# Optimization experiments

Hardware: AMD Instinct MI355X
Metric: run time of the kernel (lower is better)

The kernel has to match this reference:

```python
import jax, jax.numpy as jnp
import numpy as np
from jax.scipy.special import logsumexp

N_STATES = 64
N_OBS = 10000
BATCH = 256
T_MAX = 2048


def setup_inputs() -> dict:
    key = jax.random.key(0)
    k1, k2, k3, k4, k5 = jax.random.split(key, 5)
    x = jax.random.randint(k1, (BATCH, T_MAX), 0, N_OBS, dtype=jnp.int64 if jax.config.jax_enable_x64 else jnp.int32)
    T = jax.random.randint(k2, (BATCH,), 1, T_MAX + 1, dtype=x.dtype)  # lengths in [1, T_MAX]
    pi = jnp.zeros((N_STATES,), dtype=jnp.float32)
    unnormalized_transition_matrix = jax.random.normal(k3, (N_STATES, N_STATES), dtype=jnp.float32)
    unnormalized_emission_matrix = jax.random.normal(k4, (N_STATES, N_OBS), dtype=jnp.float32)
    return {
        "x": x,
        "T": T,
        "pi": pi,
        "unnormalized_transition_matrix": unnormalized_transition_matrix,
        "unnormalized_emission_matrix": unnormalized_emission_matrix,
    }


def reference(x, T, pi, unnormalized_transition_matrix, unnormalized_emission_matrix):
    # log p(x) via the log-domain forward algorithm.
    log_pi = jax.nn.log_softmax(pi, axis=0)                                  # [N]
    log_A = jax.nn.log_softmax(unnormalized_transition_matrix, axis=0)       # [N, N], A[i,k] = p(i | k)-style per torch dim=0
    log_E = jax.nn.log_softmax(unnormalized_emission_matrix, axis=1)         # [N, M]

    # emissions[b, t, n] = log_E[n, x[b, t]]  (gather once, not per step)
    emis = log_E.T[x]                                                        # [B, Tm, N]

    alpha0 = emis[:, 0, :] + log_pi                                          # [B, N]

    def step(alpha, e_t):
        # new_alpha[b, i] = e_t[b, i] + logsumexp_k (log_A[i, k] + alpha[b, k])
        new = e_t + logsumexp(log_A[None, :, :] + alpha[:, None, :], axis=2)
        return new, new

    _, alphas = jax.lax.scan(step, alpha0, jnp.swapaxes(emis[:, 1:, :], 0, 1))  # [Tm-1, B, N]
    log_alpha = jnp.concatenate([alpha0[None], alphas], axis=0)              # [Tm, B, N]

    log_sums = logsumexp(log_alpha, axis=2).T                                # [B, Tm]
    idx = (T - 1).astype(jnp.int32)[:, None]
    log_probs = jnp.take_along_axis(log_sums, idx, axis=1)                   # [B, 1]
    return log_probs
```

## Files before the change

kernel.cpp:

```cpp
#include <hip/hip_runtime.h>
#include <math.h>

#define NS   64
#define NOBS 10000
#define NB   256
#define TMAX 2048

#define PIP_OFF 0
#define ASW_OFF 64
#define LSE_OFF (64 + 4096)
#define ET_OFF  (64 + 4096 + 64)

__device__ __forceinline__ float wsum64(float v) {
  v += __shfl_xor(v, 1);
  v += __shfl_xor(v, 2);
  v += __shfl_xor(v, 4);
  v += __shfl_xor(v, 8);
  v += __shfl_xor(v, 16);
  v += __shfl_xor(v, 32);
  return v;
}

#define DPPROR(S, N)                                                           \
  __int_as_float(__builtin_amdgcn_update_dpp(                                  \
      0, __float_as_int(S), 0x120 + (N), 0xF, 0xF, true))

__global__ __launch_bounds__(64) void prep_small(const float* __restrict__ pi,
                                                 const float* __restrict__ A,
                                                 float* __restrict__ ws) {
  const int l = threadIdx.x;
  const int r = l & 15, c = l >> 4;
  float p = pi[l];
  float m = p;
  m = fmaxf(m, __shfl_xor(m, 1));
  m = fmaxf(m, __shfl_xor(m, 2));
  m = fmaxf(m, __shfl_xor(m, 4));
  m = fmaxf(m, __shfl_xor(m, 8));
  m = fmaxf(m, __shfl_xor(m, 16));
  m = fmaxf(m, __shfl_xor(m, 32));
  float ex = expf(p - m);
  float s = wsum64(ex);
  ws[PIP_OFF + l] = ex / s;

  __shared__ float Ap[NS * NS];
  float cm = -3.0e38f;
  for (int i = 0; i < NS; ++i) cm = fmaxf(cm, A[i * NS + l]);
  float cs = 0.f;
  for (int i = 0; i < NS; ++i) cs += expf(A[i * NS + l] - cm);
  float inv = 1.0f / cs;
  for (int i = 0; i < NS; ++i) Ap[i * NS + l] = expf(A[i * NS + l] - cm) * inv;
  __syncthreads();

  const int probe = __builtin_amdgcn_update_dpp(0, l, 0x121, 0xF, 0xF, true);
  const int dir = ((probe & 15) == ((r - 1) & 15)) ? 1 : -1;

  for (int g = 0; g < 4; ++g)
    for (int j = 0; j < 16; ++j)
      ws[ASW_OFF + l * 64 + g * 16 + j] =
          Ap[(r + 16 * g) * NS + (16 * c + ((r - dir * j) & 15))];
}

__global__ __launch_bounds__(256) void emis_lse(const float* __restrict__ E,
                                                float* __restrict__ ws) {
  const int s = blockIdx.x;
  const float* row = E + (size_t)s * NOBS;
  __shared__ float red[4];
  float m = -3.0e38f;
  for (int o = threadIdx.x; o < NOBS; o += 256) m = fmaxf(m, row[o]);
  m = fmaxf(m, __shfl_xor(m, 1));
  m = fmaxf(m, __shfl_xor(m, 2));
  m = fmaxf(m, __shfl_xor(m, 4));
  m = fmaxf(m, __shfl_xor(m, 8));
  m = fmaxf(m, __shfl_xor(m, 16));
  m = fmaxf(m, __shfl_xor(m, 32));
  const int wid = threadIdx.x >> 6;
  if ((threadIdx.x & 63) == 0) red[wid] = m;
  __syncthreads();
  m = fmaxf(fmaxf(red[0], red[1]), fmaxf(red[2], red[3]));
  __syncthreads();
  float sum = 0.f;
  for (int o = threadIdx.x; o < NOBS; o += 256) sum += expf(row[o] - m);
  sum = wsum64(sum);
  if ((threadIdx.x & 63) == 0) red[wid] = sum;
  __syncthreads();
  if (threadIdx.x == 0)
    ws[LSE_OFF + s] = m + logf(red[0] + red[1] + red[2] + red[3]);
}

__global__ __launch_bounds__(256) void emis_fill(const float* __restrict__ E,
                                                 float* __restrict__ ws) {
  const int idx = blockIdx.x * 256 + threadIdx.x;
  if (idx >= NS * NOBS) return;
  const int s = idx & 63;
  const int obs = idx >> 6;
  ws[ET_OFF + idx] = expf(E[(size_t)s * NOBS + obs] - ws[LSE_OFF + s]);
}


#define PIN8(i)                                                                \
  asm volatile("" : "+v"(aw[(i)]), "+v"(aw[(i) + 1]), "+v"(aw[(i) + 2]),       \
                    "+v"(aw[(i) + 3]), "+v"(aw[(i) + 4]), "+v"(aw[(i) + 5]),   \
                    "+v"(aw[(i) + 6]), "+v"(aw[(i) + 7]))
#define PIN_AW() do { PIN8(0); PIN8(8); PIN8(16); PIN8(24);                    \
                      PIN8(32); PIN8(40); PIN8(48); PIN8(56); } while (0)

#define STAGE_CHUNK(XS, HALF) do {                                             \
    _Pragma("unroll")                                                          \
    for (int k_ = 0; k_ < 64; ++k_) {                                          \
      const int xt_ = __builtin_amdgcn_readlane((XS), k_);                     \
      const float* gp_ = ET + ((size_t)(unsigned)xt_ << 6) + lane;             \
      __builtin_amdgcn_global_load_lds(gp_, &ebuf[(((HALF) << 6) + k_) << 6],  \
                                       4, 0, 0);                               \
    } } while (0)

#define EREAD(DST, ADDR, IMM)                                                  \
  asm volatile("ds_read_b32 %0, %1 offset:" #IMM : "=v"(DST) : "v"(ADDR))

#define STEP(u, EC) do {                                                       \
    const int t_ = t0 + (u);                                                   \
    const float e_ = EC[(u)];                                                  \
    float es_;                                                                 \
    if (((u) & 1) != 0) {               \
      const unsigned srf_ = __builtin_amdgcn_readfirstlane(__float_as_uint(s));\
      const int se_ = (int)((srf_ >> 23) & 0xFFu) - 127;                       \
      es_ = e_ * __uint_as_float((unsigned)(127 - se_) << 23);                 \
      E2 += se_;                                                               \
    } else { es_ = e_; }                                                       \
    float rot[16];                                                             \
    rot[0] = s;                                                                \
    rot[1] = DPPROR(s, 1);   rot[2] = DPPROR(s, 2);   rot[3] = DPPROR(s, 3);   \
    rot[4] = DPPROR(s, 4);   rot[5] = DPPROR(s, 5);   rot[6] = DPPROR(s, 6);   \
    rot[7] = DPPROR(s, 7);   rot[8] = DPPROR(s, 8);   rot[9] = DPPROR(s, 9);   \
    rot[10] = DPPROR(s, 10); rot[11] = DPPROR(s, 11); rot[12] = DPPROR(s, 12); \
    rot[13] = DPPROR(s, 13); rot[14] = DPPROR(s, 14); rot[15] = DPPROR(s, 15); \
    float q0a_ = 0.f, q1a_ = 0.f, q2a_ = 0.f, q3a_ = 0.f;                      \
    float q0b_ = 0.f, q1b_ = 0.f, q2b_ = 0.f, q3b_ = 0.f;                      \
    _Pragma("unroll")                                                          \
    for (int j_ = 0; j_ < 8; ++j_) {                                           \
      q0a_ = fmaf(aw[j_],      rot[j_], q0a_);                                 \
      q1a_ = fmaf(aw[16 + j_], rot[j_], q1a_);                                 \
      q2a_ = fmaf(aw[32 + j_], rot[j_], q2a_);                                 \
      q3a_ = fmaf(aw[48 + j_], rot[j_], q3a_);                                 \
      q0b_ = fmaf(aw[8 + j_],  rot[8 + j_], q0b_);                             \
      q1b_ = fmaf(aw[24 + j_], rot[8 + j_], q1b_);                             \
      q2b_ = fmaf(aw[40 + j_], rot[8 + j_], q2b_);                             \
      q3b_ = fmaf(aw[56 + j_], rot[8 + j_], q3b_);                             \
    }                                                                          \
    const float q0_ = q0a_ + q0b_;                                             \
    const float q1_ = q1a_ + q1b_;                                             \
    const float q2_ = q2a_ + q2b_;                                             \
    const float q3_ = q3a_ + q3b_;                                             \
      \
    float em_ = c1m ? q0_ : q2_;                                   \
    float en_ = c1m ? q1_ : q3_;                                   \
    float emc_, enc_;                                                          \
    asm("v_mov_b32 %0, %1" : "=v"(emc_) : "v"(em_));                           \
    asm("v_mov_b32 %0, %1" : "=v"(enc_) : "v"(en_));                           \
    asm("v_permlane32_swap_b32 %0, %1" : "+v"(em_), "+v"(emc_));               \
    asm("v_permlane32_swap_b32 %0, %1" : "+v"(en_), "+v"(enc_));               \
    const float pm_ = inA32 ? em_ : emc_;       \
    const float pn_ = inA32 ? en_ : enc_;       \
    const float ka_ = c1m ? q2_ : q0_;                  \
    const float kb_ = c1m ? q3_ : q1_;                  \
    const float ua_ = ka_ + pm_;                                               \
    const float ub_ = kb_ + pn_;                                               \
                         \
    float gv_ = c0m ? ua_ : ub_;                                               \
    float gvc_;                                                                \
    asm("v_mov_b32 %0, %1" : "=v"(gvc_) : "v"(gv_));                           \
    asm("v_permlane16_swap_b32 %0, %1" : "+v"(gv_), "+v"(gvc_));               \
    const float pg_ = inA16 ? gv_ : gvc_;         \
    const float kp_ = c0m ? ub_ : ua_;                                         \
    const float fin_ = kp_ + pg_;                                              \
    const float w_ = es_ * ((t_ == 0) ? pip : fin_);                           \
    if (t_ == Tn - 1) { vs = w_; e2s = E2; }                                   \
    s = w_;                                                                    \
  } while (0)

#define GROUP(T0, ECUR, ENXT) do {                                             \
    const int t0 = (T0);                                                       \
    { const unsigned ea_ =                                                     \
          ebase + ((unsigned)(((t0 + 4) & 127)) << 8) + ((unsigned)lane << 2); \
      EREAD(ENXT[0], ea_, 0);   EREAD(ENXT[1], ea_, 256);                      \
      EREAD(ENXT[2], ea_, 512); EREAD(ENXT[3], ea_, 768); }                    \
    asm volatile("s_waitcnt lgkmcnt(4)");                                      \
    __builtin_amdgcn_sched_barrier(0);                                         \
    STEP(0, ECUR); STEP(1, ECUR); STEP(2, ECUR); STEP(3, ECUR);                \
  } while (0)

__global__ void __attribute__((amdgpu_flat_work_group_size(64, 64)))
__attribute__((amdgpu_waves_per_eu(1, 1)))
hmm_fwd(const int* __restrict__ x, const int* __restrict__ T,
        const float* __restrict__ ws, float* __restrict__ out) {
  const int lane = threadIdx.x;
  const int b = blockIdx.x;
  const int cgrp = lane >> 4;
  const bool c0m = (cgrp & 1) != 0;
  const bool c1m = (cgrp & 2) != 0;
  const float* __restrict__ ET = ws + ET_OFF;
  const int* __restrict__ xb = x + (size_t)b * TMAX;
  const int Tn = T[b];

  __shared__ __align__(16) float ebuf[128 * 64];
  const unsigned ebase = (unsigned)(size_t)ebuf;

  bool inA32, inA16;
  {
    float qa = __int_as_float(lane), qb;
    asm("v_mov_b32 %0, %1" : "=v"(qb) : "v"(qa));
    asm("v_permlane32_swap_b32 %0, %1" : "+v"(qa), "+v"(qb));
    inA32 = (__float_as_int(qa) == (lane ^ 32));
    float pa = __int_as_float(lane), pb;
    asm("v_mov_b32 %0, %1" : "=v"(pb) : "v"(pa));
    asm("v_permlane16_swap_b32 %0, %1" : "+v"(pa), "+v"(pb));
    inA16 = (__float_as_int(pa) == (lane ^ 16));
  }

  float aw[NS];
  {
    const float4* ar = (const float4*)(ws + ASW_OFF + lane * NS);
#pragma unroll
    for (int q = 0; q < 16; ++q) {
      float4 f = ar[q];
      aw[4 * q + 0] = f.x; aw[4 * q + 1] = f.y;
      aw[4 * q + 2] = f.z; aw[4 * q + 3] = f.w;
    }
  }
  PIN_AW();

  const float pip = ws[PIP_OFF + lane];

  int xcur = xb[lane];
  STAGE_CHUNK(xcur, 0);
  int xnext = xb[64 + lane];
  asm volatile("s_waitcnt vmcnt(0)" ::: "memory");

  float eA[4], eB[4];
  {
    const unsigned ea_ = ebase + ((unsigned)lane << 2);
    EREAD(eA[0], ea_, 0);   EREAD(eA[1], ea_, 256);
    EREAD(eA[2], ea_, 512); EREAD(eA[3], ea_, 768);
  }

  float s = 1.0f;
  float vs = 0.f;
  int E2 = 0, e2s = 0;

  const int nch = (Tn + 63) >> 6;
  for (int c = 0; c < nch; ++c) {
    const int tb = c << 6;
    if (c + 1 < TMAX / 64) STAGE_CHUNK(xnext, (c + 1) & 1);
    xnext = ((c + 2) < TMAX / 64) ? xb[((c + 2) << 6) + lane] : 0;
#pragma unroll 1
    for (int gp = 0; gp < 7; ++gp) {
      GROUP(tb + (gp << 3), eA, eB);
      GROUP(tb + (gp << 3) + 4, eB, eA);
    }
    GROUP(tb + 56, eA, eB);
    asm volatile("s_waitcnt vmcnt(0)" ::: "memory");
    GROUP(tb + 60, eB, eA);
  }

  const float sf = wsum64(vs);
  if (lane == 0) {
    const double lp = (double)logf(sf) + (double)e2s * 0.6931471805599453;
    out[b] = (float)lp;
  }
}

extern "C" void kernel_launch(void* const* d_in, const int* in_sizes, int n_in,
                              void* d_out, int out_size, void* d_ws, size_t ws_size,
                              hipStream_t stream) {
  const int*   x  = (const int*)d_in[0];
  const int*   T  = (const int*)d_in[1];
  const float* pi = (const float*)d_in[2];
  const float* A  = (const float*)d_in[3];
  const float* E  = (const float*)d_in[4];
  float* out = (float*)d_out;
  float* ws  = (float*)d_ws;

  prep_small<<<1, 64, 0, stream>>>(pi, A, ws);
  emis_lse<<<NS, 256, 0, stream>>>(E, ws);
  emis_fill<<<(NS * NOBS + 255) / 256, 256, 0, stream>>>(E, ws);
  hmm_fwd<<<NB, 64, 0, stream>>>(x, T, ws, out);
}
```

Measured before the change: 399.8 us.

## Permute transition weights to drop selects, single FMA chain, rarer renormalization

Reorders the per-lane transition weight layout (row block c^m2) so the cross-lane reduction after the DPP matvec can use the partial sums directly, without the per-step select instructions. The two split FMA accumulator chains are merged into one chain per output, and the exponent renormalization now runs once per four steps instead of every other step. The t==0 case is peeled into a separate first chunk, which removes the per-step pip select. A single longer FMA chain lengthens the dependency latency, and less frequent rescaling makes overflow or underflow more likely.

```diff
diff --git a/kernel.cpp b/kernel.cpp
--- a/kernel.cpp
+++ b/kernel.cpp
@@ -54,10 +54,10 @@
   const int probe = __builtin_amdgcn_update_dpp(0, l, 0x121, 0xF, 0xF, true);
   const int dir = ((probe & 15) == ((r - 1) & 15)) ? 1 : -1;
 
-  for (int g = 0; g < 4; ++g)
+  for (int m2 = 0; m2 < 4; ++m2)
     for (int j = 0; j < 16; ++j)
-      ws[ASW_OFF + l * 64 + g * 16 + j] =
-          Ap[(r + 16 * g) * NS + (16 * c + ((r - dir * j) & 15))];
+      ws[ASW_OFF + l * 64 + m2 * 16 + j] =
+          Ap[(r + 16 * (c ^ m2)) * NS + (16 * c + ((r - dir * j) & 15))];
 }
 
 __global__ __launch_bounds__(256) void emis_lse(const float* __restrict__ E,
@@ -120,7 +120,7 @@
     const int t_ = t0 + (u);                                                   \
     const float e_ = EC[(u)];                                                  \
     float es_;                                                                 \
-    if (((u) & 1) != 0) {               \
+    if ((u) == 3) {                     \
       const unsigned srf_ = __builtin_amdgcn_readfirstlane(__float_as_uint(s));\
       const int se_ = (int)((srf_ >> 23) & 0xFFu) - 127;                       \
       es_ = e_ * __uint_as_float((unsigned)(127 - se_) << 23);                 \
@@ -133,46 +133,35 @@
     rot[7] = DPPROR(s, 7);   rot[8] = DPPROR(s, 8);   rot[9] = DPPROR(s, 9);   \
     rot[10] = DPPROR(s, 10); rot[11] = DPPROR(s, 11); rot[12] = DPPROR(s, 12); \
     rot[13] = DPPROR(s, 13); rot[14] = DPPROR(s, 14); rot[15] = DPPROR(s, 15); \
-    float q0a_ = 0.f, q1a_ = 0.f, q2a_ = 0.f, q3a_ = 0.f;                      \
-    float q0b_ = 0.f, q1b_ = 0.f, q2b_ = 0.f, q3b_ = 0.f;                      \
+         \
+    float q0_ = aw[0]  * rot[0];                                               \
+    float q1_ = aw[16] * rot[0];                                               \
+    float q2_ = aw[32] * rot[0];                                               \
+    float q3_ = aw[48] * rot[0];                                               \
     _Pragma("unroll")                                                          \
-    for (int j_ = 0; j_ < 8; ++j_) {                                           \
-      q0a_ = fmaf(aw[j_],      rot[j_], q0a_);                                 \
-      q1a_ = fmaf(aw[16 + j_], rot[j_], q1a_);                                 \
-      q2a_ = fmaf(aw[32 + j_], rot[j_], q2a_);                                 \
-      q3a_ = fmaf(aw[48 + j_], rot[j_], q3a_);                                 \
-      q0b_ = fmaf(aw[8 + j_],  rot[8 + j_], q0b_);                             \
-      q1b_ = fmaf(aw[24 + j_], rot[8 + j_], q1b_);                             \
-      q2b_ = fmaf(aw[40 + j_], rot[8 + j_], q2b_);                             \
-      q3b_ = fmaf(aw[56 + j_], rot[8 + j_], q3b_);                             \
+    for (int j_ = 1; j_ < 16; ++j_) {                                          \
+      q0_ = fmaf(aw[j_],      rot[j_], q0_);                                   \
+      q1_ = fmaf(aw[16 + j_], rot[j_], q1_);                                   \
+      q2_ = fmaf(aw[32 + j_], rot[j_], q2_);                                   \
+      q3_ = fmaf(aw[48 + j_], rot[j_], q3_);                                   \
     }                                                                          \
-    const float q0_ = q0a_ + q0b_;                                             \
-    const float q1_ = q1a_ + q1b_;                                             \
-    const float q2_ = q2a_ + q2b_;                                             \
-    const float q3_ = q3a_ + q3b_;                                             \
-      \
-    float em_ = c1m ? q0_ : q2_;                                   \
-    float en_ = c1m ? q1_ : q3_;                                   \
-    float emc_, enc_;                                                          \
-    asm("v_mov_b32 %0, %1" : "=v"(emc_) : "v"(em_));                           \
-    asm("v_mov_b32 %0, %1" : "=v"(enc_) : "v"(en_));                           \
-    asm("v_permlane32_swap_b32 %0, %1" : "+v"(em_), "+v"(emc_));               \
-    asm("v_permlane32_swap_b32 %0, %1" : "+v"(en_), "+v"(enc_));               \
-    const float pm_ = inA32 ? em_ : emc_;       \
-    const float pn_ = inA32 ? en_ : enc_;       \
-    const float ka_ = c1m ? q2_ : q0_;                  \
-    const float kb_ = c1m ? q3_ : q1_;                  \
-    const float ua_ = ka_ + pm_;                                               \
-    const float ub_ = kb_ + pn_;                                               \
-                         \
-    float gv_ = c0m ? ua_ : ub_;                                               \
-    float gvc_;                                                                \
-    asm("v_mov_b32 %0, %1" : "=v"(gvc_) : "v"(gv_));                           \
-    asm("v_permlane16_swap_b32 %0, %1" : "+v"(gv_), "+v"(gvc_));               \
-    const float pg_ = inA16 ? gv_ : gvc_;         \
-    const float kp_ = c0m ? ub_ : ua_;                                         \
-    const float fin_ = kp_ + pg_;                                              \
-    const float w_ = es_ * ((t_ == 0) ? pip : fin_);                           \
+            \
+    float t2_, t3_;                                                            \
+    asm("v_mov_b32 %0, %1" : "=v"(t2_) : "v"(q2_));                            \
+    asm("v_mov_b32 %0, %1" : "=v"(t3_) : "v"(q3_));                            \
+    asm("v_permlane32_swap_b32 %0, %1" : "+v"(q2_), "+v"(t2_));                \
+    asm("v_permlane32_swap_b32 %0, %1" : "+v"(q3_), "+v"(t3_));                \
+    const float pm_ = inA32 ? q2_ : t2_;                                       \
+    const float pn_ = inA32 ? q3_ : t3_;                                       \
+    const float ua_ = q0_ + pm_;            \
+    float ub_ = q1_ + pn_;                  \
+                  \
+    float tg_;                                                                 \
+    asm("v_mov_b32 %0, %1" : "=v"(tg_) : "v"(ub_));                            \
+    asm("v_permlane16_swap_b32 %0, %1" : "+v"(ub_), "+v"(tg_));                \
+    const float pg_ = inA16 ? ub_ : tg_;                                       \
+    const float fin_ = ua_ + pg_;                                              \
+    const float w_ = es_ * fin_;                                               \
     if (t_ == Tn - 1) { vs = w_; e2s = E2; }                                   \
     s = w_;                                                                    \
   } while (0)
@@ -188,15 +177,23 @@
     STEP(0, ECUR); STEP(1, ECUR); STEP(2, ECUR); STEP(3, ECUR);                \
   } while (0)
 
+#define GROUP_FIRST(ECUR, ENXT) do {                                           \
+    const int t0 = 0;                                                          \
+    { const unsigned ea_ =                                                     \
+          ebase + ((unsigned)4 << 8) + ((unsigned)lane << 2);                  \
+      EREAD(ENXT[0], ea_, 0);   EREAD(ENXT[1], ea_, 256);                      \
+      EREAD(ENXT[2], ea_, 512); EREAD(ENXT[3], ea_, 768); }                    \
+    asm volatile("s_waitcnt lgkmcnt(4)");                                      \
+    __builtin_amdgcn_sched_barrier(0);                                         \
+    STEP(1, ECUR); STEP(2, ECUR); STEP(3, ECUR);                               \
+  } while (0)
+
 __global__ void __attribute__((amdgpu_flat_work_group_size(64, 64)))
 __attribute__((amdgpu_waves_per_eu(1, 1)))
 hmm_fwd(const int* __restrict__ x, const int* __restrict__ T,
         const float* __restrict__ ws, float* __restrict__ out) {
   const int lane = threadIdx.x;
   const int b = blockIdx.x;
-  const int cgrp = lane >> 4;
-  const bool c0m = (cgrp & 1) != 0;
-  const bool c1m = (cgrp & 2) != 0;
   const float* __restrict__ ET = ws + ET_OFF;
   const int* __restrict__ xb = x + (size_t)b * TMAX;
   const int Tn = T[b];
@@ -241,13 +238,32 @@
     EREAD(eA[0], ea_, 0);   EREAD(eA[1], ea_, 256);
     EREAD(eA[2], ea_, 512); EREAD(eA[3], ea_, 768);
   }
-
-  float s = 1.0f;
-  float vs = 0.f;
+  asm volatile("s_waitcnt lgkmcnt(0)");
+  __builtin_amdgcn_sched_barrier(0);
+
+  float s, vs = 0.f;
   int E2 = 0, e2s = 0;
 
   const int nch = (Tn + 63) >> 6;
-  for (int c = 0; c < nch; ++c) {
+
+  {
+    if (1 < TMAX / 64) STAGE_CHUNK(xnext, 1);
+    xnext = xb[(2 << 6) + lane];
+    s = eA[0] * pip;
+    if (Tn == 1) { vs = s; e2s = 0; }
+    GROUP_FIRST(eA, eB);
+    GROUP(4, eB, eA);
+#pragma unroll 1
+    for (int gp = 1; gp < 7; ++gp) {
+      GROUP(gp << 3, eA, eB);
+      GROUP((gp << 3) + 4, eB, eA);
+    }
+    GROUP(56, eA, eB);
+    asm volatile("s_waitcnt vmcnt(0)" ::: "memory");
+    GROUP(60, eB, eA);
+  }
+
+  for (int c = 1; c < nch; ++c) {
     const int tb = c << 6;
     if (c + 1 < TMAX / 64) STAGE_CHUNK(xnext, (c + 1) & 1);
     xnext = ((c + 2) < TMAX / 64) ? xb[((c + 2) << 6) + lane] : 0;
```

New measurement: 439.3 us. 1.1x slower.
